# Kernel tuning notes

Measured on AMD Instinct MI355X. Metric: run time of the kernel, lower is better.

The kernel has to match this reference:

```python
import jax, jax.numpy as jnp
import numpy as np

B, S, T = 4, 512, 512
D, F, L, H, V = 512, 2048, 6, 8, 32000
HD = D // H


def setup_inputs() -> dict:
    key = jax.random.key(0)
    ks = list(jax.random.split(key, 16))
    it = iter(ks)

    def w(shape, scale=0.02):
        return jax.random.normal(next(it), shape, jnp.float32) * scale

    enc_in = jax.random.randint(next(it), (B, S), 0, V, dtype=jnp.int32)
    dec_in = jax.random.randint(next(it), (B, T), 0, V, dtype=jnp.int32)

    # sinusoidal positional encoding (make_sine_pos_encoding)
    pos = np.arange(S)[:, None].astype(np.float32)
    i = np.arange(D)[None, :].astype(np.float32)
    angle = pos / np.power(10000.0, (2.0 * np.floor(i / 2.0)) / D)
    pe = np.zeros((S, D), np.float32)
    pe[:, 0::2] = np.sin(angle[:, 0::2])
    pe[:, 1::2] = np.cos(angle[:, 1::2])

    return {
        "enc_in": enc_in,
        "dec_in": dec_in,
        "e_embed": w((V, D)),
        "d_embed": w((V, D)),
        "pos_enc": jnp.asarray(pe),
        "enc_mha_W": w((L, 4, D, D)),      # q,k,v,out
        "enc_mha_b": jnp.zeros((L, 4, D), jnp.float32),
        "enc_ln_g": jnp.ones((L, 2, D), jnp.float32),
        "enc_ln_b": jnp.zeros((L, 2, D), jnp.float32),
        "enc_ffn_W1": w((L, D, F)),
        "enc_ffn_b1": jnp.zeros((L, F), jnp.float32),
        "enc_ffn_W2": w((L, F, D)),
        "enc_ffn_b2": jnp.zeros((L, D), jnp.float32),
        "dec_mha_W": w((L, 8, D, D)),      # self q,k,v,out then cross q,k,v,out
        "dec_mha_b": jnp.zeros((L, 8, D), jnp.float32),
        "dec_ln_g": jnp.ones((L, 3, D), jnp.float32),
        "dec_ln_b": jnp.zeros((L, 3, D), jnp.float32),
        "dec_ffn_W1": w((L, D, F)),
        "dec_ffn_b1": jnp.zeros((L, F), jnp.float32),
        "dec_ffn_W2": w((L, F, D)),
        "dec_ffn_b2": jnp.zeros((L, D), jnp.float32),
    }


def _layer_norm(x, g, b, eps=1e-6):
    m = jnp.mean(x, axis=-1, keepdims=True)
    v = jnp.mean(jnp.square(x - m), axis=-1, keepdims=True)
    return (x - m) * jax.lax.rsqrt(v + eps) * g + b


def _split_heads(x):
    b, n, _ = x.shape
    return x.reshape(b, n, H, HD).transpose(0, 2, 1, 3)  # b h n d


def _mha(xq, xkv, W, b, mask):
    # W: [>=4, D, D] slice of (q,k,v,out); mask: broadcastable to [b,h,nq,nk]
    q = _split_heads(xq @ W[0] + b[0])
    k = _split_heads(xkv @ W[1] + b[1])
    v = _split_heads(xkv @ W[2] + b[2])
    s = jnp.einsum('bhqd,bhkd->bhqk', q, k) / jnp.sqrt(jnp.float32(HD))
    s = s + mask * (-1e9)
    a = jax.nn.softmax(s, axis=-1)
    o = jnp.einsum('bhqk,bhkd->bhqd', a, v)
    o = o.transpose(0, 2, 1, 3).reshape(xq.shape[0], xq.shape[1], D)
    return o @ W[3] + b[3]


def _forward(enc_in, dec_in, e_embed, d_embed, pos_enc,
             enc_mha_W, enc_mha_b, enc_ln_g, enc_ln_b,
             enc_ffn_W1, enc_ffn_b1, enc_ffn_W2, enc_ffn_b2,
             dec_mha_W, dec_mha_b, dec_ln_g, dec_ln_b,
             dec_ffn_W1, dec_ffn_b1, dec_ffn_W2, dec_ffn_b2):
    # masks: 1.0 where attention is blocked
    enc_pad = (enc_in == 0).astype(jnp.float32)[:, None, None, :]   # [B,1,1,S]
    dec_pad = (dec_in == 0).astype(jnp.float32)[:, None, None, :]   # [B,1,1,T]
    la = jnp.triu(jnp.ones((T, T), jnp.float32), k=1)[None, None]   # [1,1,T,T]
    look_ahead = jnp.maximum(la, dec_pad)                           # [B,1,T,T]

    scale = jnp.float32(D) ** 0.5
    e = e_embed[enc_in] * scale + pos_enc[None, :S]
    d = d_embed[dec_in] * scale + pos_enc[None, :T]

    for l in range(L):
        y = _mha(e, e, enc_mha_W[l], enc_mha_b[l], enc_pad)
        e = _layer_norm(e + y, enc_ln_g[l, 0], enc_ln_b[l, 0])
        y = jax.nn.relu(e @ enc_ffn_W1[l] + enc_ffn_b1[l]) @ enc_ffn_W2[l] + enc_ffn_b2[l]
        e = _layer_norm(e + y, enc_ln_g[l, 1], enc_ln_b[l, 1])

    for l in range(L):
        y = _mha(d, d, dec_mha_W[l, 0:4], dec_mha_b[l, 0:4], look_ahead)
        d = _layer_norm(d + y, dec_ln_g[l, 0], dec_ln_b[l, 0])
        y = _mha(d, e, dec_mha_W[l, 4:8], dec_mha_b[l, 4:8], enc_pad)
        d = _layer_norm(d + y, dec_ln_g[l, 1], dec_ln_b[l, 1])
        y = jax.nn.relu(d @ dec_ffn_W1[l] + dec_ffn_b1[l]) @ dec_ffn_W2[l] + dec_ffn_b2[l]
        d = _layer_norm(d + y, dec_ln_g[l, 2], dec_ln_b[l, 2])

    return d @ d_embed.T  # [B,T,V] logits


def reference(enc_in, dec_in, e_embed, d_embed, pos_enc,
              enc_mha_W, enc_mha_b, enc_ln_g, enc_ln_b,
              enc_ffn_W1, enc_ffn_b1, enc_ffn_W2, enc_ffn_b2,
              dec_mha_W, dec_mha_b, dec_ln_g, dec_ln_b,
              dec_ffn_W1, dec_ffn_b1, dec_ffn_W2, dec_ffn_b2):
    return _forward(enc_in, dec_in, e_embed, d_embed, pos_enc,
                    enc_mha_W, enc_mha_b, enc_ln_g, enc_ln_b,
                    enc_ffn_W1, enc_ffn_b1, enc_ffn_W2, enc_ffn_b2,
                    dec_mha_W, dec_mha_b, dec_ln_g, dec_ln_b,
                    dec_ffn_W1, dec_ffn_b1, dec_ffn_W2, dec_ffn_b2)
```

## Files before the change

kernel.cpp:

```cpp
#include <hip/hip_runtime.h>
#include <hip/hip_bf16.h>
#include <math.h>

#define B_ 4
#define S_ 512
#define D_ 512
#define F_ 2048
#define L_ 6
#define H_ 8
#define V_ 32000

typedef unsigned short u16;
typedef __attribute__((ext_vector_type(8))) short bhalf8;
typedef __attribute__((ext_vector_type(4))) float f32x4;

__device__ __forceinline__ u16 f2b(float v) {
    unsigned x = __builtin_bit_cast(unsigned, v);
    return (u16)((x + 0x7FFFu + ((x >> 16) & 1u)) >> 16);
}

#define GLD16(g, l) __builtin_amdgcn_global_load_lds( \
    (const __attribute__((address_space(1))) void*)(g), \
    (__attribute__((address_space(3))) void*)(l), 16, 0, 0)

__device__ __forceinline__ float redmax16(float v) {
    #pragma unroll
    for (int m = 1; m < 16; m <<= 1) v = fmaxf(v, __shfl_xor(v, m));
    return v;
}
__device__ __forceinline__ float redsum16(float v) {
    #pragma unroll
    for (int m = 1; m < 16; m <<= 1) v += __shfl_xor(v, m);
    return v;
}

template<int NWR, int NWC, int WM, int WN, int OUT, int RELU, int MLOOP,
         int SPLITA, int NT, int VTT, int SWZ>
__global__ __launch_bounds__(NWR * NWC * 64)
void mfma_gemm(const u16* __restrict__ A, const u16* __restrict__ A2, int acut,
               const u16* __restrict__ B,
               const float* __restrict__ bias, void* __restrict__ Cv,
               int K, int lda, int ldb, int ldc,
               u16* __restrict__ vtp, int vc0, long zoffC)
{
    constexpr int BM = NWR * WM, BN = NWC * WN;
    constexpr int NW = NWR * NWC;
    constexpr int CH_A = BM / 16, CH_B = BN / 16, CH = CH_A + CH_B;
    constexpr int NI = WM / 16, NJ = WN / 16;
    constexpr int TSTR = BM + 8;

    __shared__ u16 As[2][BM * 32];
    __shared__ u16 Bs[2][BN * 32];
    __shared__ u16 TT[VTT ? 64 * TSTR : 8];

    const int tid = threadIdx.x;
    const int wid = tid >> 6, lane = tid & 63;
    const int wrow = wid / NWC, wcol = wid % NWC;
    long bn, bmbase;
    if (SWZ) {
        long b0 = blockIdx.x;
        long per = (long)gridDim.x >> 3;
        long w = (b0 & 7) * per + (b0 >> 3);
        constexpr int MB = 16 / MLOOP;
        bn = (w / MB) * BN;
        bmbase = w % MB;
    } else {
        bn = (long)blockIdx.x * BN;
        bmbase = (long)blockIdx.y;
    }
    const int r4 = lane >> 2, c4 = lane & 3;
    const int l15 = lane & 15, l4 = lane >> 4;

    const u16* Ause = (SPLITA && bn >= acut) ? A2 : A;
    const long kz = (long)blockIdx.z * K;
    Ause += kz;
    B += kz;

    #pragma unroll 1
    for (int mi = 0; mi < MLOOP; ++mi) {
        const long bm = (bmbase * MLOOP + mi) * BM;

        f32x4 acc[NI][NJ];
        #pragma unroll
        for (int i = 0; i < NI; ++i)
            #pragma unroll
            for (int j = 0; j < NJ; ++j)
                acc[i][j] = (f32x4){0.f, 0.f, 0.f, 0.f};

        #pragma unroll
        for (int t = 0; t < CH / NW; ++t) {
            int c = wid + t * NW;
            if (c < CH_A) {
                GLD16(Ause + (bm + c * 16 + r4) * (long)lda + c4 * 8,
                      &As[0][c * 512 + lane * 8]);
            } else {
                int cb = c - CH_A;
                GLD16(B + (bn + cb * 16 + r4) * (long)ldb + c4 * 8,
                      &Bs[0][cb * 512 + lane * 8]);
            }
        }

        for (int k0 = 0; k0 < K; k0 += 32) {
            const int cur = (k0 >> 5) & 1;
            __syncthreads();
            if (k0 + 32 < K) {
                const int kn = k0 + 32;
                #pragma unroll
                for (int t = 0; t < CH / NW; ++t) {
                    int c = wid + t * NW;
                    if (c < CH_A) {
                        GLD16(Ause + (bm + c * 16 + r4) * (long)lda + kn + c4 * 8,
                              &As[cur ^ 1][c * 512 + lane * 8]);
                    } else {
                        int cb = c - CH_A;
                        GLD16(B + (bn + cb * 16 + r4) * (long)ldb + kn + c4 * 8,
                              &Bs[cur ^ 1][cb * 512 + lane * 8]);
                    }
                }
            }
            bhalf8 af[NI], bfr[NJ];
            #pragma unroll
            for (int i = 0; i < NI; ++i)
                af[i] = *(const bhalf8*)&As[cur][(wrow * WM + i * 16 + l15) * 32 + l4 * 8];
            #pragma unroll
            for (int j = 0; j < NJ; ++j)
                bfr[j] = *(const bhalf8*)&Bs[cur][(wcol * WN + j * 16 + l15) * 32 + l4 * 8];
            #pragma unroll
            for (int i = 0; i < NI; ++i)
                #pragma unroll
                for (int j = 0; j < NJ; ++j)
                    acc[i][j] = __builtin_amdgcn_mfma_f32_16x16x32_bf16(af[i], bfr[j], acc[i][j], 0, 0, 0);
        }

        if (VTT && vtp != nullptr && bn >= vc0) {
            #pragma unroll
            for (int j = 0; j < NJ; ++j) {
                const int cc = wcol * WN + j * 16 + l15;
                const float bv = bias ? bias[bn + cc] : 0.f;
                #pragma unroll
                for (int i = 0; i < NI; ++i) {
                    const int rw = wrow * WM + i * 16 + (l4 << 2);
                    #pragma unroll
                    for (int r = 0; r < 4; ++r)
                        TT[cc * TSTR + rw + r] = f2b(acc[i][j][r] + bv);
                }
            }
            __syncthreads();
            {
                const int cc = tid;
                const u16* src = &TT[cc * TSTR];
                u16* dst = &vtp[(bn - vc0 + cc) * 2048 + bm];
                #pragma unroll
                for (int p = 0; p < BM / 8; ++p)
                    *(uint4*)(dst + p * 8) = *(const uint4*)(src + p * 8);
            }
            __syncthreads();
            continue;
        }

        float* Cf = (float*)Cv + blockIdx.z * zoffC;
        u16*   Cb = (u16*)Cv  + blockIdx.z * zoffC;
        const int rowb = wrow * WM + (l4 << 2);
        const int colb = wcol * WN + l15;
        #pragma unroll
        for (int j = 0; j < NJ; ++j) {
            const long gc = bn + colb + j * 16;
            const float bv = bias ? bias[gc] : 0.f;
            #pragma unroll
            for (int i = 0; i < NI; ++i) {
                const long gr = bm + rowb + i * 16;
                #pragma unroll
                for (int r = 0; r < 4; ++r) {
                    float v = acc[i][j][r] + bv;
                    if (RELU) v = fmaxf(v, 0.f);
                    if (OUT == 0) {
                        if (NT) __builtin_nontemporal_store(v, &Cf[(gr + r) * (long)ldc + gc]);
                        else    Cf[(gr + r) * (long)ldc + gc] = v;
                    } else {
                        Cb[(gr + r) * (long)ldc + gc] = f2b(v);
                    }
                }
            }
        }
    }
}

__global__ __launch_bounds__(512)
void gemm_ln_kernel(const u16* __restrict__ A, const u16* __restrict__ B,
                    const float* __restrict__ bias,
                    float* __restrict__ x, u16* __restrict__ xb,
                    const float* __restrict__ g, const float* __restrict__ bb,
                    int K)
{
    __shared__ u16 As[16 * 32];
    __shared__ u16 Bs[512 * 32];
    __shared__ float red[2][16][8];
    __shared__ float mv[2][16];

    const int tid = threadIdx.x, w = tid >> 6, lane = tid & 63;
    const int l15 = lane & 15, l4 = lane >> 4;
    const int r4 = lane >> 2, c4 = lane & 3;
    const long bm = (long)blockIdx.x * 16;

    f32x4 acc[4];
    #pragma unroll
    for (int j = 0; j < 4; ++j) acc[j] = (f32x4){0.f, 0.f, 0.f, 0.f};

    for (int k0 = 0; k0 < K; k0 += 32) {
        #pragma unroll
        for (int t = 0; t < 5; ++t) {
            int c = w + t * 8;
            if (c < 33) {
                if (c == 0) {
                    GLD16(A + (bm + r4) * (long)K + k0 + c4 * 8, As + lane * 8);
                } else {
                    GLD16(B + ((c - 1) * 16 + r4) * (long)K + k0 + c4 * 8,
                          Bs + (c - 1) * 512 + lane * 8);
                }
            }
        }
        __syncthreads();
        bhalf8 af = *(const bhalf8*)&As[l15 * 32 + l4 * 8];
        #pragma unroll
        for (int j = 0; j < 4; ++j) {
            bhalf8 bf = *(const bhalf8*)&Bs[(w * 64 + j * 16 + l15) * 32 + l4 * 8];
            acc[j] = __builtin_amdgcn_mfma_f32_16x16x32_bf16(af, bf, acc[j], 0, 0, 0);
        }
        __syncthreads();
    }

    float vbuf[4][4], s[4] = {0, 0, 0, 0}, s2[4] = {0, 0, 0, 0};
    #pragma unroll
    for (int j = 0; j < 4; ++j) {
        int col = w * 64 + j * 16 + l15;
        float bv = bias[col];
        #pragma unroll
        for (int r = 0; r < 4; ++r) {
            int row = l4 * 4 + r;
            float v = acc[j][r] + bv + x[(bm + row) * 512 + col];
            vbuf[j][r] = v;
            s[r] += v; s2[r] += v * v;
        }
    }
    #pragma unroll
    for (int r = 0; r < 4; ++r) { s[r] = redsum16(s[r]); s2[r] = redsum16(s2[r]); }
    if (l15 == 0) {
        #pragma unroll
        for (int r = 0; r < 4; ++r) {
            red[0][l4 * 4 + r][w] = s[r];
            red[1][l4 * 4 + r][w] = s2[r];
        }
    }
    __syncthreads();
    if (tid < 16) {
        float S = 0.f, S2 = 0.f;
        #pragma unroll
        for (int q = 0; q < 8; ++q) { S += red[0][tid][q]; S2 += red[1][tid][q]; }
        float mean = S * (1.f / 512.f);
        float var = S2 * (1.f / 512.f) - mean * mean;
        mv[0][tid] = mean;
        mv[1][tid] = rsqrtf(var + 1e-6f);
    }
    __syncthreads();
    #pragma unroll
    for (int j = 0; j < 4; ++j) {
        int col = w * 64 + j * 16 + l15;
        float gg = g[col], bbv = bb[col];
        #pragma unroll
        for (int r = 0; r < 4; ++r) {
            int row = l4 * 4 + r;
            float o = (vbuf[j][r] - mv[0][row]) * mv[1][row] * gg + bbv;
            x[(bm + row) * 512 + col] = o;
            xb[(bm + row) * 512 + col] = f2b(o);
        }
    }
}

template<int CAUSAL>
__global__ __launch_bounds__(256)
void flash_kernel(const u16* __restrict__ Qp, int ldq,
                  const u16* __restrict__ Kp, int ldk,
                  const u16* __restrict__ Vt,
                  const int* __restrict__ tok,
                  u16* __restrict__ Op)
{
    __shared__ u16 QS[64 * 64];
    __shared__ u16 KS[2][64 * 64];
    __shared__ u16 VS[2][64 * 64];
    __shared__ u16 PS[4 * 16 * 64];
    __shared__ float MK[512];

    const int tid = threadIdx.x, lane = tid & 63, w = tid >> 6;
    const int l15 = lane & 15, l4 = lane >> 4;
    const int qb = blockIdx.x, bh = blockIdx.y;
    const int b = bh >> 3, h = bh & 7;

    const u16* Q = Qp + (long)(b * 512 + qb * 64) * ldq + h * 64;
    const u16* K = Kp + (long)(b * 512) * ldk + h * 64;
    const u16* V = Vt + (long)(h * 64) * 2048 + b * 512;
    u16* O = Op + (long)(b * 512 + qb * 64) * 512 + h * 64;

    {
        int t0 = tok[b * 512 + tid];
        int t1 = tok[b * 512 + 256 + tid];
        MK[tid]       = (t0 == 0) ? -1e9f : 0.f;
        MK[tid + 256] = (t1 == 0) ? -1e9f : 0.f;
    }
    const int r = tid >> 3;
    const int c = (tid & 7) ^ (r & 7);
    {
        GLD16(Q + (long)r * ldq + c * 8,        QS + tid * 8);
        GLD16(Q + (long)(r + 32) * ldq + c * 8, QS + 2048 + tid * 8);
        GLD16(K + (long)r * ldk + c * 8,              KS[0] + tid * 8);
        GLD16(K + (long)(32 + r) * ldk + c * 8,       KS[0] + 2048 + tid * 8);
        GLD16(V + (long)r * 2048 + c * 8,             VS[0] + tid * 8);
        GLD16(V + (long)(r + 32) * 2048 + c * 8,      VS[0] + 2048 + tid * 8);
    }
    __syncthreads();

    bhalf8 qa[2];
    #pragma unroll
    for (int kc = 0; kc < 2; ++kc) {
        int row = w * 16 + l15;
        qa[kc] = *(const bhalf8*)&QS[row * 64 + (((kc * 4 + l4) ^ (row & 7)) << 3)];
    }

    f32x4 oacc[4];
    float mrun[4], lrun[4];
    #pragma unroll
    for (int j = 0; j < 4; ++j) oacc[j] = (f32x4){0.f, 0.f, 0.f, 0.f};
    #pragma unroll
    for (int rr = 0; rr < 4; ++rr) { mrun[rr] = -1e30f; lrun[rr] = 0.f; }

    const int tmax = CAUSAL ? qb : 7;

    for (int t = 0; t <= tmax; ++t) {
        const int cur = t & 1;
        if (t < tmax) {
            const int tn = t + 1;
            GLD16(K + (long)(tn * 64 + r) * ldk + c * 8,        KS[cur ^ 1] + tid * 8);
            GLD16(K + (long)(tn * 64 + 32 + r) * ldk + c * 8,   KS[cur ^ 1] + 2048 + tid * 8);
            GLD16(V + (long)r * 2048 + tn * 64 + c * 8,         VS[cur ^ 1] + tid * 8);
            GLD16(V + (long)(r + 32) * 2048 + tn * 64 + c * 8,  VS[cur ^ 1] + 2048 + tid * 8);
        }
        f32x4 sac[4];
        #pragma unroll
        for (int jj = 0; jj < 4; ++jj) sac[jj] = (f32x4){0.f, 0.f, 0.f, 0.f};
        bhalf8 kf[4][2];
        #pragma unroll
        for (int jj = 0; jj < 4; ++jj)
            #pragma unroll
            for (int kc = 0; kc < 2; ++kc) {
                int row = jj * 16 + l15;
                kf[jj][kc] = *(const bhalf8*)&KS[cur][row * 64 + (((kc * 4 + l4) ^ (row & 7)) << 3)];
            }
        #pragma unroll
        for (int jj = 0; jj < 4; ++jj)
            #pragma unroll
            for (int kc = 0; kc < 2; ++kc)
                sac[jj] = __builtin_amdgcn_mfma_f32_16x16x32_bf16(qa[kc], kf[jj][kc], sac[jj], 0, 0, 0);

        #pragma unroll
        for (int jj = 0; jj < 4; ++jj) {
            float mk = MK[t * 64 + jj * 16 + l15];
            #pragma unroll
            for (int rr = 0; rr < 4; ++rr) {
                float mk2 = mk;
                if (CAUSAL && t == qb) {
                    int col = t * 64 + jj * 16 + l15;
                    int qr = qb * 64 + w * 16 + l4 * 4 + rr;
                    if (col > qr) mk2 = -1e9f;
                }
                sac[jj][rr] = sac[jj][rr] * 0.125f + mk2;
            }
        }
        #pragma unroll
        for (int rr = 0; rr < 4; ++rr) {
            float mx = fmaxf(fmaxf(sac[0][rr], sac[1][rr]), fmaxf(sac[2][rr], sac[3][rr]));
            mx = redmax16(mx);
            float mnew = fmaxf(mrun[rr], mx);
            float alpha = __expf(mrun[rr] - mnew);
            float sum = 0.f;
            int row_p = l4 * 4 + rr;
            #pragma unroll
            for (int jj = 0; jj < 4; ++jj) {
                float pv = __expf(sac[jj][rr] - mnew);
                sum += pv;
                int kv = jj * 16 + l15;
                PS[w * 1024 + row_p * 64 + ((((kv >> 3) ^ (row_p & 7)) << 3) | (kv & 7))] = f2b(pv);
            }
            sum = redsum16(sum);
            lrun[rr] = lrun[rr] * alpha + sum;
            mrun[rr] = mnew;
            #pragma unroll
            for (int jd = 0; jd < 4; ++jd) oacc[jd][rr] *= alpha;
        }
        bhalf8 pa[2], vf[4][2];
        #pragma unroll
        for (int kc = 0; kc < 2; ++kc) {
            int row = l15;
            pa[kc] = *(const bhalf8*)&PS[w * 1024 + row * 64 + (((kc * 4 + l4) ^ (row & 7)) << 3)];
        }
        #pragma unroll
        for (int jd = 0; jd < 4; ++jd)
            #pragma unroll
            for (int kc = 0; kc < 2; ++kc) {
                int row = jd * 16 + l15;
                vf[jd][kc] = *(const bhalf8*)&VS[cur][row * 64 + (((kc * 4 + l4) ^ (row & 7)) << 3)];
            }
        #pragma unroll
        for (int jd = 0; jd < 4; ++jd)
            #pragma unroll
            for (int kc = 0; kc < 2; ++kc)
                oacc[jd] = __builtin_amdgcn_mfma_f32_16x16x32_bf16(pa[kc], vf[jd][kc], oacc[jd], 0, 0, 0);
        __syncthreads();
    }

    #pragma unroll
    for (int rr = 0; rr < 4; ++rr) {
        float inv = 1.f / lrun[rr];
        int row = w * 16 + l4 * 4 + rr;
        #pragma unroll
        for (int jd = 0; jd < 4; ++jd)
            O[(long)row * 512 + jd * 16 + l15] = f2b(oacc[jd][rr] * inv);
    }
}

__global__ __launch_bounds__(256)
void transpose_many(const float* __restrict__ inA, const float* __restrict__ inB,
                    int zsplit, int R, int C, u16* __restrict__ out)
{
    int z = blockIdx.z;
    const float* in = (z < zsplit) ? inA + (long)z * R * C
                                   : inB + (long)(z - zsplit) * R * C;
    u16* o = out + (long)z * R * C;
    __shared__ float tb[64][65];
    const int tr = blockIdx.y * 64, tc = blockIdx.x * 64;
    const int col = threadIdx.x & 63, r0 = threadIdx.x >> 6;
    #pragma unroll
    for (int p = 0; p < 16; ++p) {
        int row = r0 * 16 + p;
        tb[row][col] = in[(long)(tr + row) * C + tc + col];
    }
    __syncthreads();
    #pragma unroll
    for (int p = 0; p < 16; ++p) {
        int row = r0 * 16 + p;
        o[(long)(tc + row) * R + tr + col] = f2b(tb[col][row]);
    }
}

__global__ __launch_bounds__(256)
void convert_b16(const float4* __restrict__ in, u16* __restrict__ out, long n4)
{
    long i = (long)blockIdx.x * 256 + threadIdx.x;
    if (i >= n4) return;
    float4 v = in[i];
    uint2 p;
    p.x = (unsigned)f2b(v.x) | ((unsigned)f2b(v.y) << 16);
    p.y = (unsigned)f2b(v.z) | ((unsigned)f2b(v.w) << 16);
    *(uint2*)(out + i * 4) = p;
}

__global__ __launch_bounds__(256)
void embed_kernel(const int* __restrict__ tE, const int* __restrict__ tD,
                  const float* __restrict__ eE, const float* __restrict__ eD,
                  const float* __restrict__ pos,
                  float* __restrict__ xE, float* __restrict__ xD,
                  u16* __restrict__ bE, u16* __restrict__ bD, float scale)
{
    const int z = blockIdx.y;
    const int* tok = z ? tD : tE;
    const float* emb = z ? eD : eE;
    float* x = z ? xD : xE;
    u16* xb = z ? bD : bE;
    int row = blockIdx.x;
    int s = row & (S_ - 1);
    int t = tok[row];
    const float* er = emb + (long)t * D_;
    const float* pr = pos + (long)s * D_;
    float* o = x + (long)row * D_;
    u16*  ob = xb + (long)row * D_;
    int i = threadIdx.x;
    float v0 = er[i]       * scale + pr[i];
    float v1 = er[i + 256] * scale + pr[i + 256];
    o[i] = v0;        o[i + 256] = v1;
    ob[i] = f2b(v0);  ob[i + 256] = f2b(v1);
}

__global__ __launch_bounds__(256)
void add_ln_kernel(float* __restrict__ x, const float* __restrict__ y0,
                   const float* __restrict__ y1, const float* __restrict__ cb,
                   u16* __restrict__ xb,
                   const float* __restrict__ g, const float* __restrict__ bb)
{
    long row = blockIdx.x;
    float* xr = x + row * D_;
    u16* xo = xb + row * D_;
    const float* yr0 = y0 + row * D_;
    const float* yr1 = y1 + row * D_;
    int t = threadIdx.x, t2 = t + 256;

    float r0 = xr[t]  + yr0[t]  + yr1[t]  + cb[t];
    float r1 = xr[t2] + yr0[t2] + yr1[t2] + cb[t2];
    float s = r0 + r1;
    float s2 = r0 * r0 + r1 * r1;
    #pragma unroll
    for (int i = 1; i < 64; i <<= 1) {
        s  += __shfl_xor(s, i);
        s2 += __shfl_xor(s2, i);
    }
    __shared__ float rs[4], rs2[4];
    int wid = t >> 6;
    if ((t & 63) == 0) { rs[wid] = s; rs2[wid] = s2; }
    __syncthreads();
    s  = rs[0] + rs[1] + rs[2] + rs[3];
    s2 = rs2[0] + rs2[1] + rs2[2] + rs2[3];

    float mean = s * (1.f / D_);
    float var  = s2 * (1.f / D_) - mean * mean;
    float inv  = rsqrtf(var + 1e-6f);
    float o0 = (r0 - mean) * inv * g[t]  + bb[t];
    float o1 = (r1 - mean) * inv * g[t2] + bb[t2];
    xr[t] = o0;       xr[t2] = o1;
    xo[t] = f2b(o0);  xo[t2] = f2b(o1);
}

extern "C" void kernel_launch(void* const* d_in, const int* in_sizes, int n_in,
                              void* d_out, int out_size, void* d_ws, size_t ws_size,
                              hipStream_t stream)
{
    const int*   enc_in     = (const int*)  d_in[0];
    const int*   dec_in     = (const int*)  d_in[1];
    const float* e_embed    = (const float*)d_in[2];
    const float* d_embed    = (const float*)d_in[3];
    const float* pos_enc    = (const float*)d_in[4];
    const float* enc_mha_W  = (const float*)d_in[5];
    const float* enc_mha_b  = (const float*)d_in[6];
    const float* enc_ln_g   = (const float*)d_in[7];
    const float* enc_ln_b   = (const float*)d_in[8];
    const float* enc_ffn_W1 = (const float*)d_in[9];
    const float* enc_ffn_b1 = (const float*)d_in[10];
    const float* enc_ffn_W2 = (const float*)d_in[11];
    const float* enc_ffn_b2 = (const float*)d_in[12];
    const float* dec_mha_W  = (const float*)d_in[13];
    const float* dec_mha_b  = (const float*)d_in[14];
    const float* dec_ln_g   = (const float*)d_in[15];
    const float* dec_ln_b   = (const float*)d_in[16];
    const float* dec_ffn_W1 = (const float*)d_in[17];
    const float* dec_ffn_b1 = (const float*)d_in[18];
    const float* dec_ffn_W2 = (const float*)d_in[19];
    const float* dec_ffn_b2 = (const float*)d_in[20];
    float* out = (float*)d_out;

    const int  BS  = B_ * S_;
    const long BSD = (long)BS * D_;
    const long DD  = (long)D_ * D_;
    const long DF  = (long)D_ * F_;

    char* p = (char*)d_ws;
    auto alloc = [&](long bytes) { char* r = p; p += (bytes + 255) & ~255L; return r; };
    float* e    = (float*)alloc(BSD * 4);
    float* dd   = (float*)alloc(BSD * 4);
    float* y    = (float*)alloc(2 * BSD * 4);
    u16*   eb   = (u16*)  alloc(BSD * 2);
    u16*   ddb  = (u16*)  alloc(BSD * 2);
    u16*   qkv  = (u16*)  alloc((long)BS * 1536 * 2);
    u16*   att  = (u16*)  alloc(BSD * 2);
    u16*   vt   = (u16*)  alloc(BSD * 2);
    u16*   ffnh = (u16*)  alloc((long)BS * F_ * 2);
    u16*   wEmb = (u16*)  alloc((long)V_ * D_ * 2);
    u16*   wMha = (u16*)  alloc(72 * DD * 2);
    u16*   wF1  = (u16*)  alloc(12 * DF * 2);
    u16*   wF2  = (u16*)  alloc(12 * DF * 2);

    transpose_many<<<dim3(8, 8, 72), 256, 0, stream>>>(enc_mha_W, dec_mha_W, 24, 512, 512, wMha);
    transpose_many<<<dim3(32, 8, 12), 256, 0, stream>>>(enc_ffn_W1, dec_ffn_W1, 6, 512, 2048, wF1);
    transpose_many<<<dim3(8, 32, 12), 256, 0, stream>>>(enc_ffn_W2, dec_ffn_W2, 6, 2048, 512, wF2);
    convert_b16<<<16000, 256, 0, stream>>>((const float4*)d_embed, wEmb, (long)V_ * D_ / 4);

    const float scale = sqrtf((float)D_);
    embed_kernel<<<dim3(BS, 2), 256, 0, stream>>>(enc_in, dec_in, e_embed, d_embed,
                                                  pos_enc, e, dd, eb, ddb, scale);

    #define GEMM_SKV(A, Bp, bias, C) \
        mfma_gemm<1,1,32,64,1,0,1,0,0,1,0><<<dim3(24, 64), 64, 0, stream>>>( \
            A, A, 1 << 30, Bp, bias, C, 512, 512, 512, 1536, vt, 1024, 0)
    #define GEMM_FFN1(A, Bp, bias, C) \
        mfma_gemm<1,1,32,64,1,1,1,0,0,0,0><<<dim3(32, 64), 64, 0, stream>>>( \
            A, A, 1 << 30, Bp, bias, C, 512, 512, 512, 2048, nullptr, 0, 0)
    #define GEMM_FFN2(A, Bp) \
        mfma_gemm<2,1,32,64,0,0,1,0,0,0,0><<<dim3(8, 32, 2), 128, 0, stream>>>( \
            A, A, 1 << 30, Bp, nullptr, y, 1024, 2048, 2048, 512, nullptr, 0, BSD)

    for (int l = 0; l < L_; ++l) {
        const u16* Wl = wMha + (long)l * 4 * DD;
        const float* bl = enc_mha_b + (long)l * 4 * D_;
        GEMM_SKV(eb, Wl, bl, qkv);
        flash_kernel<0><<<dim3(8, 32), 256, 0, stream>>>(qkv, 1536, qkv + 512, 1536, vt, enc_in, att);
        gemm_ln_kernel<<<128, 512, 0, stream>>>(att, Wl + 3 * DD, bl + 3 * D_,
            e, eb, enc_ln_g + (long)(l * 2) * D_, enc_ln_b + (long)(l * 2) * D_, 512);
        GEMM_FFN1(eb, wF1 + (long)l * DF, enc_ffn_b1 + (long)l * F_, ffnh);
        GEMM_FFN2(ffnh, wF2 + (long)l * DF);
        add_ln_kernel<<<BS, 256, 0, stream>>>(e, y, y + BSD, enc_ffn_b2 + (long)l * D_, eb,
            enc_ln_g + (long)(l * 2 + 1) * D_, enc_ln_b + (long)(l * 2 + 1) * D_);
    }

    for (int l = 0; l < L_; ++l) {
        const u16* Wl = wMha + (long)(24 + l * 8) * DD;
        const float* bl = dec_mha_b + (long)l * 8 * D_;
        GEMM_SKV(ddb, Wl, bl, qkv);
        flash_kernel<1><<<dim3(8, 32), 256, 0, stream>>>(qkv, 1536, qkv + 512, 1536, vt, dec_in, att);
        gemm_ln_kernel<<<128, 512, 0, stream>>>(att, Wl + 3 * DD, bl + 3 * D_,
            dd, ddb, dec_ln_g + (long)(l * 3) * D_, dec_ln_b + (long)(l * 3) * D_, 512);
        mfma_gemm<1,1,32,64,1,0,1,1,0,1,0><<<dim3(24, 64), 64, 0, stream>>>(
            ddb, eb, 512, Wl + 4 * DD, bl + 4 * D_, qkv,
            512, 512, 512, 1536, vt, 1024, 0);
        flash_kernel<0><<<dim3(8, 32), 256, 0, stream>>>(qkv, 1536, qkv + 512, 1536, vt, enc_in, att);
        gemm_ln_kernel<<<128, 512, 0, stream>>>(att, Wl + 7 * DD, bl + 7 * D_,
            dd, ddb, dec_ln_g + (long)(l * 3 + 1) * D_, dec_ln_b + (long)(l * 3 + 1) * D_, 512);
        GEMM_FFN1(ddb, wF1 + (long)(6 + l) * DF, dec_ffn_b1 + (long)l * F_, ffnh);
        GEMM_FFN2(ffnh, wF2 + (long)(6 + l) * DF);
        add_ln_kernel<<<BS, 256, 0, stream>>>(dd, y, y + BSD, dec_ffn_b2 + (long)l * D_, ddb,
            dec_ln_g + (long)(l * 3 + 2) * D_, dec_ln_b + (long)(l * 3 + 2) * D_);
    }

    mfma_gemm<2,2,64,64,0,0,2,0,1,0,1><<<dim3(2000), 256, 0, stream>>>(
        ddb, ddb, 1 << 30, wEmb, nullptr, out, 512, 512, 512, 32000, nullptr, 0, 0);
}
```

Measured before the change: 1.660 ms.

## Fuse FFN2 GEMM with residual LayerNorm, double-buffer gemm_ln, add MFMA priority

Replaces the split-K FFN2 GEMM plus separate add_ln kernel with one kernel. Each block writes its partial tile, then the last block to finish a row tile, found through an atomic counter, does the residual add and LayerNorm. The gemm_ln kernel now double-buffers its LDS tiles so the next K slice loads while the current one computes. The flash attention MFMA sections get s_setprio hints, and the final logits GEMM uses a different tile parameter with half the grid. This saves one launch per layer and some global traffic, at the cost of a serialized LN tail in the last-arriving block and counter-reset bookkeeping.

```diff
diff --git a/kernel.cpp b/kernel.cpp
--- a/kernel.cpp
+++ b/kernel.cpp
@@ -192,8 +192,8 @@
                     const float* __restrict__ g, const float* __restrict__ bb,
                     int K)
 {
-    __shared__ u16 As[16 * 32];
-    __shared__ u16 Bs[512 * 32];
+    __shared__ u16 As[2][16 * 32];
+    __shared__ u16 Bs[2][512 * 32];
     __shared__ float red[2][16][8];
     __shared__ float mv[2][16];
 
@@ -206,27 +206,38 @@
     #pragma unroll
     for (int j = 0; j < 4; ++j) acc[j] = (f32x4){0.f, 0.f, 0.f, 0.f};
 
+    #pragma unroll
+    for (int t = 0; t < 5; ++t) {
+        int c = w + t * 8;
+        if (c < 33) {
+            if (c == 0) GLD16(A + (bm + r4) * (long)K + c4 * 8, As[0] + lane * 8);
+            else        GLD16(B + ((c - 1) * 16 + r4) * (long)K + c4 * 8,
+                              Bs[0] + (c - 1) * 512 + lane * 8);
+        }
+    }
+
     for (int k0 = 0; k0 < K; k0 += 32) {
-        #pragma unroll
-        for (int t = 0; t < 5; ++t) {
-            int c = w + t * 8;
-            if (c < 33) {
-                if (c == 0) {
-                    GLD16(A + (bm + r4) * (long)K + k0 + c4 * 8, As + lane * 8);
-                } else {
-                    GLD16(B + ((c - 1) * 16 + r4) * (long)K + k0 + c4 * 8,
-                          Bs + (c - 1) * 512 + lane * 8);
+        const int cur = (k0 >> 5) & 1;
+        __syncthreads();
+        if (k0 + 32 < K) {
+            const int kn = k0 + 32;
+            #pragma unroll
+            for (int t = 0; t < 5; ++t) {
+                int c = w + t * 8;
+                if (c < 33) {
+                    if (c == 0) GLD16(A + (bm + r4) * (long)K + kn + c4 * 8,
+                                      As[cur ^ 1] + lane * 8);
+                    else        GLD16(B + ((c - 1) * 16 + r4) * (long)K + kn + c4 * 8,
+                                      Bs[cur ^ 1] + (c - 1) * 512 + lane * 8);
                 }
             }
         }
-        __syncthreads();
-        bhalf8 af = *(const bhalf8*)&As[l15 * 32 + l4 * 8];
+        bhalf8 af = *(const bhalf8*)&As[cur][l15 * 32 + l4 * 8];
         #pragma unroll
         for (int j = 0; j < 4; ++j) {
-            bhalf8 bf = *(const bhalf8*)&Bs[(w * 64 + j * 16 + l15) * 32 + l4 * 8];
+            bhalf8 bf = *(const bhalf8*)&Bs[cur][(w * 64 + j * 16 + l15) * 32 + l4 * 8];
             acc[j] = __builtin_amdgcn_mfma_f32_16x16x32_bf16(af, bf, acc[j], 0, 0, 0);
         }
-        __syncthreads();
     }
 
     float vbuf[4][4], s[4] = {0, 0, 0, 0}, s2[4] = {0, 0, 0, 0};
@@ -272,6 +283,133 @@
             float o = (vbuf[j][r] - mv[0][row]) * mv[1][row] * gg + bbv;
             x[(bm + row) * 512 + col] = o;
             xb[(bm + row) * 512 + col] = f2b(o);
+        }
+    }
+}
+
+__global__ __launch_bounds__(128)
+void ffn2_ln_kernel(const u16* __restrict__ A, const u16* __restrict__ B,
+                    float* __restrict__ y, long zoff,
+                    const float* __restrict__ cb,
+                    float* __restrict__ x, u16* __restrict__ xb,
+                    const float* __restrict__ g, const float* __restrict__ bb,
+                    int* __restrict__ cnt)
+{
+    __shared__ u16 As[2][64 * 32];
+    __shared__ u16 Bs[2][64 * 32];
+    __shared__ int lastFlag;
+
+    const int tid = threadIdx.x;
+    const int wid = tid >> 6, lane = tid & 63;
+    const long bn = (long)blockIdx.x * 64;
+    const long bm = (long)blockIdx.y * 64;
+    const int r4 = lane >> 2, c4 = lane & 3;
+    const int l15 = lane & 15, l4 = lane >> 4;
+    const int K = 1024, lda = 2048, ldb = 2048;
+    const u16* Ap = A + (long)blockIdx.z * K;
+    const u16* Bp = B + (long)blockIdx.z * K;
+
+    f32x4 acc[2][4];
+    #pragma unroll
+    for (int i = 0; i < 2; ++i)
+        #pragma unroll
+        for (int j = 0; j < 4; ++j) acc[i][j] = (f32x4){0.f, 0.f, 0.f, 0.f};
+
+    #pragma unroll
+    for (int t = 0; t < 4; ++t) {
+        int c = wid + t * 2;
+        if (c < 4) GLD16(Ap + (bm + c * 16 + r4) * (long)lda + c4 * 8,
+                         &As[0][c * 512 + lane * 8]);
+        else { int cb2 = c - 4;
+               GLD16(Bp + (bn + cb2 * 16 + r4) * (long)ldb + c4 * 8,
+                     &Bs[0][cb2 * 512 + lane * 8]); }
+    }
+    for (int k0 = 0; k0 < K; k0 += 32) {
+        const int cur = (k0 >> 5) & 1;
+        __syncthreads();
+        if (k0 + 32 < K) {
+            const int kn = k0 + 32;
+            #pragma unroll
+            for (int t = 0; t < 4; ++t) {
+                int c = wid + t * 2;
+                if (c < 4) GLD16(Ap + (bm + c * 16 + r4) * (long)lda + kn + c4 * 8,
+                                 &As[cur ^ 1][c * 512 + lane * 8]);
+                else { int cb2 = c - 4;
+                       GLD16(Bp + (bn + cb2 * 16 + r4) * (long)ldb + kn + c4 * 8,
+                             &Bs[cur ^ 1][cb2 * 512 + lane * 8]); }
+            }
+        }
+        bhalf8 af[2], bfr[4];
+        #pragma unroll
+        for (int i = 0; i < 2; ++i)
+            af[i] = *(const bhalf8*)&As[cur][(wid * 32 + i * 16 + l15) * 32 + l4 * 8];
+        #pragma unroll
+        for (int j = 0; j < 4; ++j)
+            bfr[j] = *(const bhalf8*)&Bs[cur][(j * 16 + l15) * 32 + l4 * 8];
+        #pragma unroll
+        for (int i = 0; i < 2; ++i)
+            #pragma unroll
+            for (int j = 0; j < 4; ++j)
+                acc[i][j] = __builtin_amdgcn_mfma_f32_16x16x32_bf16(af[i], bfr[j], acc[i][j], 0, 0, 0);
+    }
+
+    float* Y = y + blockIdx.z * zoff;
+    const int rowb = wid * 32 + (l4 << 2);
+    #pragma unroll
+    for (int j = 0; j < 4; ++j) {
+        const long gc = bn + l15 + j * 16;
+        #pragma unroll
+        for (int i = 0; i < 2; ++i) {
+            const long gr = bm + rowb + i * 16;
+            #pragma unroll
+            for (int r = 0; r < 4; ++r)
+                Y[(gr + r) * 512 + gc] = acc[i][j][r];
+        }
+    }
+    __threadfence();
+    if (tid == 0) {
+        int old = atomicAdd(&cnt[blockIdx.y], 1);
+        lastFlag = (old == 15);
+    }
+    __syncthreads();
+    if (!lastFlag) return;
+    __threadfence();
+    if (tid == 0) cnt[blockIdx.y] = 0;
+
+    const float* y0 = y;
+    const float* y1 = y + zoff;
+    for (int rr = 0; rr < 32; ++rr) {
+        const long row = bm + wid * 32 + rr;
+        const float* xr = x  + row * 512;
+        const float* a0 = y0 + row * 512;
+        const float* a1 = y1 + row * 512;
+        float v[8]; float s = 0.f, s2 = 0.f;
+        #pragma unroll
+        for (int q = 0; q < 2; ++q) {
+            float4 xv = *(const float4*)(xr + lane * 8 + q * 4);
+            float4 p0 = *(const float4*)(a0 + lane * 8 + q * 4);
+            float4 p1 = *(const float4*)(a1 + lane * 8 + q * 4);
+            float4 bv = *(const float4*)(cb + lane * 8 + q * 4);
+            v[q*4+0] = xv.x + p0.x + p1.x + bv.x;
+            v[q*4+1] = xv.y + p0.y + p1.y + bv.y;
+            v[q*4+2] = xv.z + p0.z + p1.z + bv.z;
+            v[q*4+3] = xv.w + p0.w + p1.w + bv.w;
+        }
+        #pragma unroll
+        for (int q = 0; q < 8; ++q) { s += v[q]; s2 += v[q] * v[q]; }
+        #pragma unroll
+        for (int m = 1; m < 64; m <<= 1) { s += __shfl_xor(s, m); s2 += __shfl_xor(s2, m); }
+        float mean = s * (1.f / 512.f);
+        float var  = s2 * (1.f / 512.f) - mean * mean;
+        float inv  = rsqrtf(var + 1e-6f);
+        float* xw = x + row * 512;
+        u16*   xo = xb + row * 512;
+        #pragma unroll
+        for (int q = 0; q < 8; ++q) {
+            int colq = lane * 8 + q;
+            float o = (v[q] - mean) * inv * g[colq] + bb[colq];
+            xw[colq] = o;
+            xo[colq] = f2b(o);
         }
     }
 }
@@ -354,11 +492,13 @@
                 int row = jj * 16 + l15;
                 kf[jj][kc] = *(const bhalf8*)&KS[cur][row * 64 + (((kc * 4 + l4) ^ (row & 7)) << 3)];
             }
+        __builtin_amdgcn_s_setprio(1);
         #pragma unroll
         for (int jj = 0; jj < 4; ++jj)
             #pragma unroll
             for (int kc = 0; kc < 2; ++kc)
                 sac[jj] = __builtin_amdgcn_mfma_f32_16x16x32_bf16(qa[kc], kf[jj][kc], sac[jj], 0, 0, 0);
+        __builtin_amdgcn_s_setprio(0);
 
         #pragma unroll
         for (int jj = 0; jj < 4; ++jj) {
@@ -408,11 +548,13 @@
                 int row = jd * 16 + l15;
                 vf[jd][kc] = *(const bhalf8*)&VS[cur][row * 64 + (((kc * 4 + l4) ^ (row & 7)) << 3)];
             }
+        __builtin_amdgcn_s_setprio(1);
         #pragma unroll
         for (int jd = 0; jd < 4; ++jd)
             #pragma unroll
             for (int kc = 0; kc < 2; ++kc)
                 oacc[jd] = __builtin_amdgcn_mfma_f32_16x16x32_bf16(pa[kc], vf[jd][kc], oacc[jd], 0, 0, 0);
+        __builtin_amdgcn_s_setprio(0);
         __syncthreads();
     }
 
@@ -486,44 +628,6 @@
     float v1 = er[i + 256] * scale + pr[i + 256];
     o[i] = v0;        o[i + 256] = v1;
     ob[i] = f2b(v0);  ob[i + 256] = f2b(v1);
-}
-
-__global__ __launch_bounds__(256)
-void add_ln_kernel(float* __restrict__ x, const float* __restrict__ y0,
-                   const float* __restrict__ y1, const float* __restrict__ cb,
-                   u16* __restrict__ xb,
-                   const float* __restrict__ g, const float* __restrict__ bb)
-{
-    long row = blockIdx.x;
-    float* xr = x + row * D_;
-    u16* xo = xb + row * D_;
-    const float* yr0 = y0 + row * D_;
-    const float* yr1 = y1 + row * D_;
-    int t = threadIdx.x, t2 = t + 256;
-
-    float r0 = xr[t]  + yr0[t]  + yr1[t]  + cb[t];
-    float r1 = xr[t2] + yr0[t2] + yr1[t2] + cb[t2];
-    float s = r0 + r1;
-    float s2 = r0 * r0 + r1 * r1;
-    #pragma unroll
-    for (int i = 1; i < 64; i <<= 1) {
-        s  += __shfl_xor(s, i);
-        s2 += __shfl_xor(s2, i);
-    }
-    __shared__ float rs[4], rs2[4];
-    int wid = t >> 6;
-    if ((t & 63) == 0) { rs[wid] = s; rs2[wid] = s2; }
-    __syncthreads();
-    s  = rs[0] + rs[1] + rs[2] + rs[3];
-    s2 = rs2[0] + rs2[1] + rs2[2] + rs2[3];
-
-    float mean = s * (1.f / D_);
-    float var  = s2 * (1.f / D_) - mean * mean;
-    float inv  = rsqrtf(var + 1e-6f);
-    float o0 = (r0 - mean) * inv * g[t]  + bb[t];
-    float o1 = (r1 - mean) * inv * g[t2] + bb[t2];
-    xr[t] = o0;       xr[t2] = o1;
-    xo[t] = f2b(o0);  xo[t2] = f2b(o1);
 }
 
 extern "C" void kernel_launch(void* const* d_in, const int* in_sizes, int n_in,
@@ -563,6 +667,7 @@
     float* e    = (float*)alloc(BSD * 4);
     float* dd   = (float*)alloc(BSD * 4);
     float* y    = (float*)alloc(2 * BSD * 4);
+    int*   cnt  = (int*)  alloc(32 * 4);
     u16*   eb   = (u16*)  alloc(BSD * 2);
     u16*   ddb  = (u16*)  alloc(BSD * 2);
     u16*   qkv  = (u16*)  alloc((long)BS * 1536 * 2);
@@ -574,6 +679,8 @@
     u16*   wF1  = (u16*)  alloc(12 * DF * 2);
     u16*   wF2  = (u16*)  alloc(12 * DF * 2);
 
+    hipMemsetAsync(cnt, 0, 32 * sizeof(int), stream);
+
     transpose_many<<<dim3(8, 8, 72), 256, 0, stream>>>(enc_mha_W, dec_mha_W, 24, 512, 512, wMha);
     transpose_many<<<dim3(32, 8, 12), 256, 0, stream>>>(enc_ffn_W1, dec_ffn_W1, 6, 512, 2048, wF1);
     transpose_many<<<dim3(8, 32, 12), 256, 0, stream>>>(enc_ffn_W2, dec_ffn_W2, 6, 2048, 512, wF2);
@@ -589,9 +696,9 @@
     #define GEMM_FFN1(A, Bp, bias, C) \
         mfma_gemm<1,1,32,64,1,1,1,0,0,0,0><<<dim3(32, 64), 64, 0, stream>>>( \
             A, A, 1 << 30, Bp, bias, C, 512, 512, 512, 2048, nullptr, 0, 0)
-    #define GEMM_FFN2(A, Bp) \
-        mfma_gemm<2,1,32,64,0,0,1,0,0,0,0><<<dim3(8, 32, 2), 128, 0, stream>>>( \
-            A, A, 1 << 30, Bp, nullptr, y, 1024, 2048, 2048, 512, nullptr, 0, BSD)
+    #define FFN2_LN(A, Bp, b2p, xs, xbs, gp, bp) \
+        ffn2_ln_kernel<<<dim3(8, 32, 2), 128, 0, stream>>>( \
+            A, Bp, y, BSD, b2p, xs, xbs, gp, bp, cnt)
 
     for (int l = 0; l < L_; ++l) {
         const u16* Wl = wMha + (long)l * 4 * DD;
@@ -601,9 +708,8 @@
         gemm_ln_kernel<<<128, 512, 0, stream>>>(att, Wl + 3 * DD, bl + 3 * D_,
             e, eb, enc_ln_g + (long)(l * 2) * D_, enc_ln_b + (long)(l * 2) * D_, 512);
         GEMM_FFN1(eb, wF1 + (long)l * DF, enc_ffn_b1 + (long)l * F_, ffnh);
-        GEMM_FFN2(ffnh, wF2 + (long)l * DF);
-        add_ln_kernel<<<BS, 256, 0, stream>>>(e, y, y + BSD, enc_ffn_b2 + (long)l * D_, eb,
-            enc_ln_g + (long)(l * 2 + 1) * D_, enc_ln_b + (long)(l * 2 + 1) * D_);
+        FFN2_LN(ffnh, wF2 + (long)l * DF, enc_ffn_b2 + (long)l * D_, e, eb,
+                enc_ln_g + (long)(l * 2 + 1) * D_, enc_ln_b + (long)(l * 2 + 1) * D_);
     }
 
     for (int l = 0; l < L_; ++l) {
@@ -620,11 +726,10 @@
         gemm_ln_kernel<<<128, 512, 0, stream>>>(att, Wl + 7 * DD, bl + 7 * D_,
             dd, ddb, dec_ln_g + (long)(l * 3 + 1) * D_, dec_ln_b + (long)(l * 3 + 1) * D_, 512);
         GEMM_FFN1(ddb, wF1 + (long)(6 + l) * DF, dec_ffn_b1 + (long)l * F_, ffnh);
-        GEMM_FFN2(ffnh, wF2 + (long)(6 + l) * DF);
-        add_ln_kernel<<<BS, 256, 0, stream>>>(dd, y, y + BSD, dec_ffn_b2 + (long)l * D_, ddb,
-            dec_ln_g + (long)(l * 3 + 2) * D_, dec_ln_b + (long)(l * 3 + 2) * D_);
-    }
-
-    mfma_gemm<2,2,64,64,0,0,2,0,1,0,1><<<dim3(2000), 256, 0, stream>>>(
+        FFN2_LN(ffnh, wF2 + (long)(6 + l) * DF, dec_ffn_b2 + (long)l * D_, dd, ddb,
+                dec_ln_g + (long)(l * 3 + 2) * D_, dec_ln_b + (long)(l * 3 + 2) * D_);
+    }
+
+    mfma_gemm<2,2,64,64,0,0,4,0,1,0,1><<<dim3(1000), 256, 0, stream>>>(
         ddb, ddb, 1 << 30, wEmb, nullptr, out, 512, 512, 512, 32000, nullptr, 0, 0);
 }
```

Measured after the change: 2.252 ms. 35.6% more time.
